# Performance work log

Measured on AMD Instinct MI355X. Metric: run time of the kernel, lower is better.

The kernel has to match this reference:

```python
import jax, jax.numpy as jnp
import numpy as np

EMBED_DIM = 1024
NUM_HEADS = 16
HEAD_DIM = EMBED_DIM // NUM_HEADS


def setup_inputs() -> dict:
    key = jax.random.key(0)
    ks = jax.random.split(key, 9)
    s = 1.0 / np.sqrt(EMBED_DIM)
    x = jax.random.normal(ks[0], (2, 2048, EMBED_DIM), dtype=jnp.float32)
    Wq = jax.random.uniform(ks[1], (EMBED_DIM, EMBED_DIM), jnp.float32, -s, s)
    bq = jax.random.uniform(ks[2], (EMBED_DIM,), jnp.float32, -s, s)
    Wk = jax.random.uniform(ks[3], (EMBED_DIM, EMBED_DIM), jnp.float32, -s, s)
    bk = jax.random.uniform(ks[4], (EMBED_DIM,), jnp.float32, -s, s)
    Wv = jax.random.uniform(ks[5], (EMBED_DIM, EMBED_DIM), jnp.float32, -s, s)
    bv = jax.random.uniform(ks[6], (EMBED_DIM,), jnp.float32, -s, s)
    Wo = jax.random.uniform(ks[7], (EMBED_DIM, EMBED_DIM), jnp.float32, -s, s)
    bo = jax.random.uniform(ks[8], (EMBED_DIM,), jnp.float32, -s, s)
    return {"x": x, "Wq": Wq, "bq": bq, "Wk": Wk, "bk": bk,
            "Wv": Wv, "bv": bv, "Wo": Wo, "bo": bo}


def reference(x, Wq, bq, Wk, bk, Wv, bv, Wo, bo):
    B, N, C = x.shape
    H, D = NUM_HEADS, HEAD_DIM
    # nn.Linear: y = x @ W.T + b; here W stored as [in, out] so y = x @ W + b
    def split_heads(y):
        return y.reshape(B, N, H, D).transpose(0, 2, 1, 3)  # [B,H,N,D]
    q = split_heads(x @ Wq + bq)
    k = split_heads(x @ Wk + bk)
    v = split_heads(x @ Wv + bv)
    scores = jnp.einsum('bhnd,bhmd->bhnm', q, k) / jnp.sqrt(jnp.float32(D)).astype(x.dtype)
    attn = jax.nn.softmax(scores, axis=-1)
    ctx = jnp.einsum('bhnm,bhmd->bhnd', attn, v)
    ctx = ctx.transpose(0, 2, 1, 3).reshape(B, N, C)
    return ctx @ Wo + bo
```

## Files before the change

kernel.cpp:

```cpp
#include <hip/hip_runtime.h>
#include <hip/hip_bf16.h>
#include <stdint.h>
#include <stddef.h>

using bf16 = __hip_bfloat16;
using bf16x8 = __attribute__((ext_vector_type(8))) short;
using f32x4  = __attribute__((ext_vector_type(4))) float;
using f32x16 = __attribute__((ext_vector_type(16))) float;
typedef unsigned int u32x2 __attribute__((ext_vector_type(2)));
typedef unsigned int u32x4 __attribute__((ext_vector_type(4)));

#define MFMA16(a, b, c) __builtin_amdgcn_mfma_f32_16x16x32_bf16((a), (b), (c), 0, 0, 0)
#define MFMA32(a, b, c) __builtin_amdgcn_mfma_f32_32x32x16_bf16((a), (b), (c), 0, 0, 0)

#define GLD16(g, l)                                                            \
  __builtin_amdgcn_global_load_lds(                                            \
      (const __attribute__((address_space(1))) void*)(g),                      \
      (__attribute__((address_space(3))) void*)(l), 16, 0, 0)

__device__ __forceinline__ float exp2_fast(float x) {
#if __has_builtin(__builtin_amdgcn_exp2f)
  return __builtin_amdgcn_exp2f(x);
#else
  return __expf(x * 0.69314718056f);
#endif
}

__device__ __forceinline__ float fmax3(float a, float b, float c) {
  return fmaxf(fmaxf(a, b), c);
}

__device__ __forceinline__ unsigned int cvtpk_bf16(float lo, float hi) {
  unsigned int r;
  asm("v_cvt_pk_bf16_f32 %0, %1, %2" : "=v"(r) : "v"(lo), "v"(hi));
  return r;
}

__device__ __forceinline__ void permswap(unsigned int& a, unsigned int& b, int hi) {
#if __has_builtin(__builtin_amdgcn_permlane32_swap)
  u32x2 r = __builtin_amdgcn_permlane32_swap(a, b, false, false);
  a = r.x;
  b = r.y;
#else
  unsigned int sa = __shfl_xor((unsigned int)a, 32, 64);
  unsigned int sb = __shfl_xor((unsigned int)b, 32, 64);
  unsigned int an = hi ? sb : a;
  unsigned int bn = hi ? b : sa;
  a = an; b = bn;
#endif
}


__global__ void convert_x(const float* __restrict__ x, bf16* __restrict__ out) {
  const int i = blockIdx.x * 256 + threadIdx.x;
  const float4 v = ((const float4*)x)[i];
  __hip_bfloat162* o2 = (__hip_bfloat162*)(out + (size_t)i * 4);
  o2[0] = __float22bfloat162_rn(make_float2(v.x, v.y));
  o2[1] = __float22bfloat162_rn(make_float2(v.z, v.w));
}

__global__ void convert_w(const float* __restrict__ W0, const float* __restrict__ W1,
                          const float* __restrict__ W2, const float* __restrict__ W3,
                          bf16* __restrict__ Wt) {
  __shared__ float t[32][33];
  const int bx = blockIdx.x;
  const int mat = bx >> 10;
  const float* W = (mat == 0) ? W0 : (mat == 1) ? W1 : (mat == 2) ? W2 : W3;
  const int rem = bx & 1023;
  const int k0 = (rem >> 5) * 32, n0 = (rem & 31) * 32;
  const int c = threadIdx.x & 31, r0 = (threadIdx.x >> 5) * 4;
#pragma unroll
  for (int i = 0; i < 4; ++i) {
    const int r = r0 + i;
    t[r][c] = W[(size_t)(k0 + r) * 1024 + n0 + c];
  }
  __syncthreads();
  bf16* dst = Wt + (size_t)mat * 1024 * 1024;
#pragma unroll
  for (int i = 0; i < 4; ++i) {
    const int rn = r0 + i;
    dst[(size_t)(n0 + rn) * 1024 + k0 + c] = __float2bfloat16(t[c][rn]);
  }
}

__global__ void concat_bias(const float* __restrict__ bq, const float* __restrict__ bk,
                            const float* __restrict__ bv, const float* __restrict__ bo,
                            float* __restrict__ dst) {
  const int i = blockIdx.x * 256 + threadIdx.x;
  const float* src = (i < 1024) ? bq : (i < 2048) ? bk : (i < 3072) ? bv : bo;
  dst[i] = src[i & 1023];
}

__global__ __launch_bounds__(512, 2)
void gemm_qkv(const bf16* __restrict__ A, const bf16* __restrict__ Bt,
              const float* __restrict__ bias,
              bf16* __restrict__ Qb, bf16* __restrict__ Kf, bf16* __restrict__ Vf) {
  __shared__ bf16 Ab[2][128 * 64];
  __shared__ bf16 Bb[2][384 * 64];
  const int tid = threadIdx.x;
  const int lane = tid & 63, w = tid >> 6;
  const int wr = w >> 2, wc = w & 3;
  const int lrow = lane & 15, lgk = lane >> 4;

  const int bid = blockIdx.x;
  const int xcd = bid & 7, i5 = bid >> 3;
  const int xr = xcd >> 1, xc = xcd & 1;
  const int bm = (xr * 8 + (i5 & 7)) * 128;
  const int bn = (xc * 4 + (i5 >> 3)) * 384;

  f32x4 acc[4][6] = {};

  auto stageA = [&](int b, int kt) {
#pragma unroll
    for (int v = 0; v < 2; ++v) {
      const int c = v * 512 + tid;
      const int r = c >> 3, j = c & 7;
      GLD16(A + (size_t)(bm + r) * 1024 + kt * 64 + ((j ^ (r & 7)) * 8),
            &Ab[b][c * 8]);
    }
  };
  auto stageB = [&](int b, int kt, int u) {
#pragma unroll
    for (int v = 0; v < 2; ++v) {
      const int cl = v * 512 + tid;
      const int r = u * 128 + (cl >> 3), j = cl & 7;
      GLD16(Bt + (size_t)(bn + r) * 1024 + kt * 64 + ((j ^ ((r & 7))) * 8),
            &Bb[b][(r * 8 + (j)) * 8]);
    }
  };

  auto readA = [&](int b, bf16x8 (&dst)[8]) {
#pragma unroll
    for (int mf = 0; mf < 4; ++mf)
#pragma unroll
      for (int kk = 0; kk < 2; ++kk) {
        const int r = wr * 64 + mf * 16 + lrow;
        const int s = (kk * 4 + lgk) ^ (r & 7);
        dst[mf * 2 + kk] = *(const bf16x8*)(&Ab[b][(r * 8 + s) * 8]);
      }
  };
  auto readB2 = [&](int b, int nf0, bf16x8 (&dst)[4]) {
#pragma unroll
    for (int nf = 0; nf < 2; ++nf)
#pragma unroll
      for (int kk = 0; kk < 2; ++kk) {
        const int r = wc * 96 + (nf0 + nf) * 16 + lrow;
        const int s = (kk * 4 + lgk) ^ (r & 7);
        dst[nf * 2 + kk] = *(const bf16x8*)(&Bb[b][(r * 8 + s) * 8]);
      }
  };

  stageA(0, 0);
  stageB(0, 0, 0);
  stageB(0, 0, 1);
  stageB(0, 0, 2);
  stageA(1, 1);
  asm volatile("s_waitcnt vmcnt(2)" ::: "memory");
  __builtin_amdgcn_s_barrier();

  bf16x8 a_[8], b01[4], b23[4], b45[4];

  for (int t = 0; t < 16; ++t) {
    const int b = t & 1, nb = b ^ 1;
    if (t < 15) {
      stageB(nb, t + 1, 0);
      stageB(nb, t + 1, 1);
    }
    readA(b, a_);
    readB2(b, 0, b01);
    asm volatile("s_waitcnt lgkmcnt(0)" ::: "memory");
    __builtin_amdgcn_sched_barrier(0);
    __builtin_amdgcn_s_setprio(1);
#pragma unroll
    for (int mf = 0; mf < 4; ++mf)
#pragma unroll
      for (int nf = 0; nf < 2; ++nf)
#pragma unroll
        for (int kk = 0; kk < 2; ++kk)
          acc[mf][nf] = MFMA16(a_[mf * 2 + kk], b01[nf * 2 + kk], acc[mf][nf]);
    __builtin_amdgcn_s_setprio(0);
    if (t < 15) stageB(nb, t + 1, 2);
    readB2(b, 2, b23);
    asm volatile("s_waitcnt lgkmcnt(0)" ::: "memory");
    __builtin_amdgcn_sched_barrier(0);
    __builtin_amdgcn_s_setprio(1);
#pragma unroll
    for (int mf = 0; mf < 4; ++mf)
#pragma unroll
      for (int nf = 0; nf < 2; ++nf)
#pragma unroll
        for (int kk = 0; kk < 2; ++kk)
          acc[mf][2 + nf] = MFMA16(a_[mf * 2 + kk], b23[nf * 2 + kk], acc[mf][2 + nf]);
    __builtin_amdgcn_s_setprio(0);
    readB2(b, 4, b45);
    asm volatile("s_waitcnt lgkmcnt(0)" ::: "memory");
    __builtin_amdgcn_sched_barrier(0);
    __builtin_amdgcn_s_barrier();
    if (t < 14) stageA(b, t + 2);
    __builtin_amdgcn_s_setprio(1);
#pragma unroll
    for (int mf = 0; mf < 4; ++mf)
#pragma unroll
      for (int nf = 0; nf < 2; ++nf)
#pragma unroll
        for (int kk = 0; kk < 2; ++kk)
          acc[mf][4 + nf] = MFMA16(a_[mf * 2 + kk], b45[nf * 2 + kk], acc[mf][4 + nf]);
    __builtin_amdgcn_s_setprio(0);
    if (t < 14)
      asm volatile("s_waitcnt vmcnt(2)" ::: "memory");
    else
      asm volatile("s_waitcnt vmcnt(0)" ::: "memory");
    __builtin_amdgcn_s_barrier();
  }

#pragma unroll
  for (int mf = 0; mf < 4; ++mf) {
#pragma unroll
    for (int nf = 0; nf < 6; ++nf) {
      const int col = bn + wc * 96 + nf * 16 + lrow;
      const float bv_ = bias[col];
      const int row0 = bm + wr * 64 + mf * 16 + lgk * 4;
      const int which = col >> 10;
      const int hd = col & 1023;
      const int h = hd >> 6, d = hd & 63;
      const int bb = row0 >> 11, t0 = row0 & 2047;
      const int bh = bb * 16 + h;
      const int tt = (t0 >> 6) & 31;
      if (which == 2) {
        const int ks = (t0 >> 4) & 3, vhi = (t0 >> 3) & 1, e0 = t0 & 7;
        const int dt = d >> 5, lo5 = d & 31;
        bf16* vp = Vf + (((size_t)bh * 32 + tt) * 8 + dt * 4 + ks) * 512 +
                   (vhi * 32 + lo5) * 8 + e0;
        uint2 pk;
        pk.x = cvtpk_bf16(acc[mf][nf][0] + bv_, acc[mf][nf][1] + bv_);
        pk.y = cvtpk_bf16(acc[mf][nf][2] + bv_, acc[mf][nf][3] + bv_);
        *(uint2*)vp = pk;
      } else if (which == 0) {
#pragma unroll
        for (int j = 0; j < 4; ++j)
          Qb[((size_t)bh * 2048 + t0 + j) * 64 + d] =
              __float2bfloat16((acc[mf][nf][j] + bv_) * 0.18033688f);
      } else {
        const int kt = (t0 >> 5) & 1, lo5 = t0 & 31;
        const int f = d >> 4, khi = (d >> 3) & 1, e = d & 7;
        bf16* kp = Kf + (((size_t)bh * 32 + tt) * 8 + kt * 4 + f) * 512 +
                   (khi * 32 + lo5) * 8 + e;
#pragma unroll
        for (int j = 0; j < 4; ++j)
          kp[j * 8] = __float2bfloat16(acc[mf][nf][j] + bv_);
      }
    }
  }
}

__global__ __launch_bounds__(256)
void gemm_o(const bf16* __restrict__ A, const bf16* __restrict__ Bt,
            const float* __restrict__ bias, float* __restrict__ Of, int K) {
  __shared__ bf16 As[3][128 * 32];
  __shared__ bf16 Bs[3][64 * 32];
  const int tid = threadIdx.x;
  const int lane = tid & 63, w = tid >> 6;
  const int wr = w >> 1, wc = w & 1;
  const int lrow = lane & 15, lgk = lane >> 4;
  const int bm = blockIdx.y * 128, bn = blockIdx.x * 64;
  f32x4 acc[4][2] = {};
  const bf16* Ab = A + (size_t)bm * K;
  const bf16* Bb = Bt + (size_t)bn * K;
  const int e0 = tid, e1 = 256 + tid;
  const int NT = K >> 5;

  auto stage = [&](int s, int k0) {
    GLD16(Ab + (size_t)(e0 >> 2) * K + k0 + (e0 & 3) * 8, &As[s][e0 * 8]);
    GLD16(Ab + (size_t)(e1 >> 2) * K + k0 + (e1 & 3) * 8, &As[s][e1 * 8]);
    GLD16(Bb + (size_t)(e0 >> 2) * K + k0 + (e0 & 3) * 8, &Bs[s][e0 * 8]);
  };

  stage(0, 0);
  stage(1, 32);
  int cur = 0, nxt = 2;
  for (int t = 0; t < NT; ++t) {
    if (t < NT - 1)
      asm volatile("s_waitcnt vmcnt(3)" ::: "memory");
    else
      asm volatile("s_waitcnt vmcnt(0)" ::: "memory");
    __builtin_amdgcn_s_barrier();
    if (t + 2 < NT) {
      stage(nxt, (t + 2) << 5);
      nxt = (nxt == 2) ? 0 : nxt + 1;
    }
    bf16x8 af[4], bfr[2];
#pragma unroll
    for (int m = 0; m < 4; ++m)
      af[m] = *(const bf16x8*)(&As[cur][(wr * 64 + m * 16 + lrow) * 32 + lgk * 8]);
#pragma unroll
    for (int n = 0; n < 2; ++n)
      bfr[n] = *(const bf16x8*)(&Bs[cur][(wc * 32 + n * 16 + lrow) * 32 + lgk * 8]);
#pragma unroll
    for (int m = 0; m < 4; ++m)
#pragma unroll
      for (int n = 0; n < 2; ++n)
        acc[m][n] = MFMA16(af[m], bfr[n], acc[m][n]);
    cur = (cur == 2) ? 0 : cur + 1;
  }

#pragma unroll
  for (int m = 0; m < 4; ++m) {
#pragma unroll
    for (int n = 0; n < 2; ++n) {
      const int col = bn + wc * 32 + n * 16 + lrow;
      const float bv_ = bias[col];
      const int row0 = bm + wr * 64 + m * 16 + lgk * 4;
#pragma unroll
      for (int j = 0; j < 4; ++j)
        Of[(size_t)(row0 + j) * 1024 + col] = acc[m][n][j] + bv_;
    }
  }
}

__global__ __launch_bounds__(256, 2)
void attn_kernel(const bf16* __restrict__ Q, const bf16* __restrict__ Kf,
                 const bf16* __restrict__ Vf, bf16* __restrict__ ctx) {
  const int tid = threadIdx.x, lane = tid & 63, w = tid >> 6;
  const int lo5 = lane & 31, hi = lane >> 5;

  const int bid = blockIdx.x;
  const int xcd = bid & 7, idx = bid >> 3;
  const int bh = (xcd << 2) | (idx >> 4);
  const int qt = idx & 15;
  const int q0 = qt * 128 + w * 32;

  const bf16* Qbh = Q + (size_t)bh * 2048 * 64;
  const bf16* Kp = Kf + (size_t)bh * 32 * 4096 + lane * 8;
  const bf16* Vp = Vf + (size_t)bh * 32 * 4096 + lane * 8;

  bf16x8 qf[4];
#pragma unroll
  for (int f = 0; f < 4; ++f)
    qf[f] = *(const bf16x8*)(Qbh + (size_t)(q0 + lo5) * 64 + f * 16 + hi * 8);

  f32x16 o0 = {}, o1 = {};
  float m2 = -1e30f;
  float lsum = 0.f;
  bf16x8 pa[4];

  auto softmax_pa = [&](f32x16& s0, f32x16& s1) {
    float r1[11];
#pragma unroll
    for (int i = 0; i < 5; ++i)
      r1[i] = fmax3(s0[3 * i], s0[3 * i + 1], s0[3 * i + 2]);
    r1[5] = fmax3(s0[15], s1[0], s1[1]);
#pragma unroll
    for (int i = 0; i < 4; ++i)
      r1[6 + i] = fmax3(s1[2 + 3 * i], s1[3 + 3 * i], s1[4 + 3 * i]);
    r1[10] = fmaxf(s1[14], s1[15]);
    float r2[4];
#pragma unroll
    for (int i = 0; i < 3; ++i) r2[i] = fmax3(r1[3 * i], r1[3 * i + 1], r1[3 * i + 2]);
    r2[3] = fmaxf(r1[9], r1[10]);
    const float pm = fmaxf(fmax3(r2[0], r2[1], r2[2]), r2[3]);
    if (!__all(pm <= m2 + 11.5416f)) {
      const float mx = fmaxf(pm, __shfl_xor(pm, 32, 64));
      const float mn = fmaxf(m2, mx);
      const float corr = exp2_fast(m2 - mn);
      m2 = mn;
      lsum *= corr;
#pragma unroll
      for (int j = 0; j < 16; ++j) { o0[j] *= corr; o1[j] *= corr; }
    }
#pragma unroll
    for (int j = 0; j < 16; ++j) s0[j] = exp2_fast(s0[j] - m2);
#pragma unroll
    for (int j = 0; j < 16; ++j) s1[j] = exp2_fast(s1[j] - m2);
    float a8[8];
#pragma unroll
    for (int j = 0; j < 8; ++j) a8[j] = (s0[j] + s0[j + 8]) + (s1[j] + s1[j + 8]);
    float a4[4];
#pragma unroll
    for (int j = 0; j < 4; ++j) a4[j] = a8[j] + a8[j + 4];
    lsum += (a4[0] + a4[1]) + (a4[2] + a4[3]);
#pragma unroll
    for (int ks = 0; ks < 4; ++ks) {
      const f32x16& s = (ks < 2) ? s0 : s1;
      const int b0 = (ks & 1) * 8;
      unsigned int a0 = cvtpk_bf16(s[b0 + 0], s[b0 + 1]);
      unsigned int c0 = cvtpk_bf16(s[b0 + 4], s[b0 + 5]);
      unsigned int a1 = cvtpk_bf16(s[b0 + 2], s[b0 + 3]);
      unsigned int c1 = cvtpk_bf16(s[b0 + 6], s[b0 + 7]);
      permswap(a0, c0, hi);
      permswap(a1, c1, hi);
      u32x4 tt;
      tt.x = a0; tt.y = a1; tt.z = c0; tt.w = c1;
      pa[ks] = __builtin_bit_cast(bf16x8, tt);
    }
  };

  bf16x8 kA[8], kB[8], vb[8];

  auto loadK = [&](int t, bf16x8 (&kb)[8]) {
    const bf16* p = Kp + (size_t)t * 4096;
#pragma unroll
    for (int fi = 0; fi < 8; ++fi) kb[fi] = *(const bf16x8*)(p + fi * 512);
  };
  auto loadV = [&](int t) {
    const bf16* p = Vp + (size_t)t * 4096;
#pragma unroll
    for (int fi = 0; fi < 8; ++fi) vb[fi] = *(const bf16x8*)(p + fi * 512);
  };

  loadK(0, kA);

  auto step = [&](int t, bf16x8 (&kc)[8], bf16x8 (&kn)[8]) {
    loadV(t);
    if (t < 31) loadK(t + 1, kn);
    f32x16 s0 = {}, s1 = {};
#pragma unroll
    for (int f = 0; f < 4; ++f) s0 = MFMA32(kc[f], qf[f], s0);
#pragma unroll
    for (int f = 0; f < 4; ++f) s1 = MFMA32(kc[4 + f], qf[f], s1);
    softmax_pa(s0, s1);
#pragma unroll
    for (int ks = 0; ks < 4; ++ks) {
      o0 = MFMA32(vb[ks], pa[ks], o0);
      o1 = MFMA32(vb[4 + ks], pa[ks], o1);
    }
  };

  for (int t = 0; t < 32; t += 2) {
    step(t, kA, kB);
    step(t + 1, kB, kA);
  }

  lsum += __shfl_xor(lsum, 32, 64);
  const float inv = 1.f / lsum;
  const int b = bh >> 4, h = bh & 15;
  bf16* crow = ctx + (size_t)(b * 2048 + q0 + lo5) * 1024 + h * 64;
#pragma unroll
  for (int g = 0; g < 4; ++g) {
    uint2 pk0, pk1;
    pk0.x = cvtpk_bf16(o0[4 * g + 0] * inv, o0[4 * g + 1] * inv);
    pk0.y = cvtpk_bf16(o0[4 * g + 2] * inv, o0[4 * g + 3] * inv);
    pk1.x = cvtpk_bf16(o1[4 * g + 0] * inv, o1[4 * g + 1] * inv);
    pk1.y = cvtpk_bf16(o1[4 * g + 2] * inv, o1[4 * g + 3] * inv);
    *(uint2*)(crow + 8 * g + 4 * hi) = pk0;
    *(uint2*)(crow + 32 + 8 * g + 4 * hi) = pk1;
  }
}


extern "C" void kernel_launch(void* const* d_in, const int* in_sizes, int n_in,
                              void* d_out, int out_size, void* d_ws, size_t ws_size,
                              hipStream_t stream) {
  const float* x  = (const float*)d_in[0];
  const float* Wq = (const float*)d_in[1];
  const float* bq = (const float*)d_in[2];
  const float* Wk = (const float*)d_in[3];
  const float* bk = (const float*)d_in[4];
  const float* Wv = (const float*)d_in[5];
  const float* bv = (const float*)d_in[6];
  const float* Wo = (const float*)d_in[7];
  const float* bo = (const float*)d_in[8];
  float* out = (float*)d_out;

  char* ws = (char*)d_ws;
  bf16* xb  = (bf16*)(ws);
  bf16* Wt  = (bf16*)(ws + ((size_t)8 << 20));
  bf16* Qb  = (bf16*)(ws + ((size_t)16 << 20));
  bf16* Kf  = (bf16*)(ws + ((size_t)24 << 20));
  bf16* Vf  = (bf16*)(ws + ((size_t)32 << 20));
  bf16* ctx = (bf16*)(ws + ((size_t)40 << 20));
  float* ba = (float*)(ws + ((size_t)48 << 20));

  convert_x<<<dim3(4096), dim3(256), 0, stream>>>(x, xb);
  convert_w<<<dim3(4096), dim3(256), 0, stream>>>(Wq, Wk, Wv, Wo, Wt);
  concat_bias<<<dim3(16), dim3(256), 0, stream>>>(bq, bk, bv, bo, ba);

  gemm_qkv<<<dim3(256), dim3(512), 0, stream>>>(xb, Wt, ba, Qb, Kf, Vf);

  attn_kernel<<<dim3(512), dim3(256), 0, stream>>>(Qb, Kf, Vf, ctx);

  gemm_o<<<dim3(16, 32), dim3(256), 0, stream>>>(
      ctx, Wt + (size_t)3072 * 1024, ba + 3072, out, 1024);
}
```

Baseline: 122.8 us.

## Split attention KV loop across two wave teams with LDS softmax merge

The attention kernel now runs 8 waves per block. Two teams of four waves each process half of the key/value tiles for the same query rows. Team 1 writes its partial output, running max and sum to shared memory, and team 0 merges them with flash-style rescaling before writing the context. This doubles parallelism per block to hide the latency of the serial KV loop. The cost is about 35KB of LDS per block, a block barrier, and tighter register limits from launch_bounds(512,4).

```diff
diff --git a/kernel.cpp b/kernel.cpp
--- a/kernel.cpp
+++ b/kernel.cpp
@@ -317,21 +317,25 @@
   }
 }
 
-__global__ __launch_bounds__(256, 2)
+__global__ __launch_bounds__(512, 4)
 void attn_kernel(const bf16* __restrict__ Q, const bf16* __restrict__ Kf,
                  const bf16* __restrict__ Vf, bf16* __restrict__ ctx) {
+  __shared__ float mbuf[4][64][34];
+
   const int tid = threadIdx.x, lane = tid & 63, w = tid >> 6;
   const int lo5 = lane & 31, hi = lane >> 5;
+  const int team = w >> 2, wq = w & 3;
 
   const int bid = blockIdx.x;
   const int xcd = bid & 7, idx = bid >> 3;
   const int bh = (xcd << 2) | (idx >> 4);
   const int qt = idx & 15;
-  const int q0 = qt * 128 + w * 32;
+  const int q0 = qt * 128 + wq * 32;
 
   const bf16* Qbh = Q + (size_t)bh * 2048 * 64;
   const bf16* Kp = Kf + (size_t)bh * 32 * 4096 + lane * 8;
   const bf16* Vp = Vf + (size_t)bh * 32 * 4096 + lane * 8;
+  const int tg0 = team * 16;
 
   bf16x8 qf[4];
 #pragma unroll
@@ -407,11 +411,11 @@
     for (int fi = 0; fi < 8; ++fi) vb[fi] = *(const bf16x8*)(p + fi * 512);
   };
 
-  loadK(0, kA);
+  loadK(tg0, kA);
 
   auto step = [&](int t, bf16x8 (&kc)[8], bf16x8 (&kn)[8]) {
-    loadV(t);
-    if (t < 31) loadK(t + 1, kn);
+    loadV(tg0 + t);
+    if (t < 15) loadK(tg0 + t + 1, kn);
     f32x16 s0 = {}, s1 = {};
 #pragma unroll
     for (int f = 0; f < 4; ++f) s0 = MFMA32(kc[f], qf[f], s0);
@@ -425,24 +429,46 @@
     }
   };
 
-  for (int t = 0; t < 32; t += 2) {
+  for (int t = 0; t < 16; t += 2) {
     step(t, kA, kB);
     step(t + 1, kB, kA);
   }
 
-  lsum += __shfl_xor(lsum, 32, 64);
-  const float inv = 1.f / lsum;
-  const int b = bh >> 4, h = bh & 15;
-  bf16* crow = ctx + (size_t)(b * 2048 + q0 + lo5) * 1024 + h * 64;
-#pragma unroll
-  for (int g = 0; g < 4; ++g) {
-    uint2 pk0, pk1;
-    pk0.x = cvtpk_bf16(o0[4 * g + 0] * inv, o0[4 * g + 1] * inv);
-    pk0.y = cvtpk_bf16(o0[4 * g + 2] * inv, o0[4 * g + 3] * inv);
-    pk1.x = cvtpk_bf16(o1[4 * g + 0] * inv, o1[4 * g + 1] * inv);
-    pk1.y = cvtpk_bf16(o1[4 * g + 2] * inv, o1[4 * g + 3] * inv);
-    *(uint2*)(crow + 8 * g + 4 * hi) = pk0;
-    *(uint2*)(crow + 32 + 8 * g + 4 * hi) = pk1;
+  if (team == 1) {
+    float* dst = &mbuf[wq][lane][0];
+#pragma unroll
+    for (int j = 0; j < 16; ++j) dst[j] = o0[j];
+#pragma unroll
+    for (int j = 0; j < 16; ++j) dst[16 + j] = o1[j];
+    dst[32] = m2;
+    dst[33] = lsum;
+  }
+  __syncthreads();
+  if (team == 0) {
+    const float* src = &mbuf[wq][lane][0];
+    const float m2B = src[32], lB = src[33];
+    const float m = fmaxf(m2, m2B);
+    const float cA = exp2_fast(m2 - m), cB = exp2_fast(m2B - m);
+    lsum = lsum * cA + lB * cB;
+#pragma unroll
+    for (int j = 0; j < 16; ++j) o0[j] = o0[j] * cA + src[j] * cB;
+#pragma unroll
+    for (int j = 0; j < 16; ++j) o1[j] = o1[j] * cA + src[16 + j] * cB;
+
+    lsum += __shfl_xor(lsum, 32, 64);
+    const float inv = 1.f / lsum;
+    const int b = bh >> 4, h = bh & 15;
+    bf16* crow = ctx + (size_t)(b * 2048 + q0 + lo5) * 1024 + h * 64;
+#pragma unroll
+    for (int g = 0; g < 4; ++g) {
+      uint2 pk0, pk1;
+      pk0.x = cvtpk_bf16(o0[4 * g + 0] * inv, o0[4 * g + 1] * inv);
+      pk0.y = cvtpk_bf16(o0[4 * g + 2] * inv, o0[4 * g + 3] * inv);
+      pk1.x = cvtpk_bf16(o1[4 * g + 0] * inv, o1[4 * g + 1] * inv);
+      pk1.y = cvtpk_bf16(o1[4 * g + 2] * inv, o1[4 * g + 3] * inv);
+      *(uint2*)(crow + 8 * g + 4 * hi) = pk0;
+      *(uint2*)(crow + 32 + 8 * g + 4 * hi) = pk1;
+    }
   }
 }
 
@@ -476,7 +502,7 @@
 
   gemm_qkv<<<dim3(256), dim3(512), 0, stream>>>(xb, Wt, ba, Qb, Kf, Vf);
 
-  attn_kernel<<<dim3(512), dim3(256), 0, stream>>>(Qb, Kf, Vf, ctx);
+  attn_kernel<<<dim3(512), dim3(512), 0, stream>>>(Qb, Kf, Vf, ctx);
 
   gemm_o<<<dim3(16, 32), dim3(256), 0, stream>>>(
       ctx, Wt + (size_t)3072 * 1024, ba + 3072, out, 1024);
```

Result: slower. 300.9 us (+145.0%).

## Double-buffer K and V tiles with inline-asm loads and manual vmcnt waits

Applied to the files above, without the earlier changes.

Attention K/V loads now go through inline-asm global_load_dwordx4, two tiles ahead, with double buffers for both K and V. Explicit s_waitcnt vmcnt counts and sched barriers replace the compiler's waits, so the loads for tile t+2 are issued after tile t is consumed. Before, V was loaded in the same step that used it, which exposed load latency. This raises register pressure (four tile buffers), so the launch bound drops the min-blocks-per-CU hint, which may lower occupancy. Hand-written waitcnt is also fragile if the compiler emits other memory ops.

```diff
diff --git a/kernel.cpp b/kernel.cpp
--- a/kernel.cpp
+++ b/kernel.cpp
@@ -317,7 +317,7 @@
   }
 }
 
-__global__ __launch_bounds__(256, 2)
+__global__ __launch_bounds__(256)
 void attn_kernel(const bf16* __restrict__ Q, const bf16* __restrict__ Kf,
                  const bf16* __restrict__ Vf, bf16* __restrict__ ctx) {
   const int tid = threadIdx.x, lane = tid & 63, w = tid >> 6;
@@ -329,14 +329,58 @@
   const int qt = idx & 15;
   const int q0 = qt * 128 + w * 32;
 
-  const bf16* Qbh = Q + (size_t)bh * 2048 * 64;
+  const bf16* Qp = Q + (size_t)bh * 2048 * 64 + (size_t)(q0 + lo5) * 64 + hi * 8;
   const bf16* Kp = Kf + (size_t)bh * 32 * 4096 + lane * 8;
   const bf16* Vp = Vf + (size_t)bh * 32 * 4096 + lane * 8;
 
   bf16x8 qf[4];
-#pragma unroll
-  for (int f = 0; f < 4; ++f)
-    qf[f] = *(const bf16x8*)(Qbh + (size_t)(q0 + lo5) * 64 + f * 16 + hi * 8);
+  asm volatile(
+      "global_load_dwordx4 %0, %4, off\n\t"
+      "global_load_dwordx4 %1, %4, off offset:32\n\t"
+      "global_load_dwordx4 %2, %4, off offset:64\n\t"
+      "global_load_dwordx4 %3, %4, off offset:96"
+      : "=v"(qf[0]), "=v"(qf[1]), "=v"(qf[2]), "=v"(qf[3])
+      : "v"(Qp)
+      : "memory");
+
+  bf16x8 kA[8], vA[8], kB[8], vB[8];
+
+#define ISSUE_TILE(t, kb, vbuf_)                                               \
+  {                                                                            \
+    const bf16* pk = Kp + (size_t)(t) * 4096;                                  \
+    const bf16* pv = Vp + (size_t)(t) * 4096;                                  \
+    asm volatile(                                                              \
+        "global_load_dwordx4 %0, %8, off\n\t"                                  \
+        "global_load_dwordx4 %1, %8, off offset:1024\n\t"                      \
+        "global_load_dwordx4 %2, %8, off offset:2048\n\t"                      \
+        "global_load_dwordx4 %3, %8, off offset:3072\n\t"                      \
+        "global_load_dwordx4 %4, %9, off\n\t"                                  \
+        "global_load_dwordx4 %5, %9, off offset:1024\n\t"                      \
+        "global_load_dwordx4 %6, %9, off offset:2048\n\t"                      \
+        "global_load_dwordx4 %7, %9, off offset:3072"                          \
+        : "=v"(kb[0]), "=v"(kb[1]), "=v"(kb[2]), "=v"(kb[3]),                  \
+          "=v"(kb[4]), "=v"(kb[5]), "=v"(kb[6]), "=v"(kb[7])                   \
+        : "v"(pk), "v"(pk + 2048)                                              \
+        : "memory");                                                           \
+    asm volatile(                                                              \
+        "global_load_dwordx4 %0, %8, off\n\t"                                  \
+        "global_load_dwordx4 %1, %8, off offset:1024\n\t"                      \
+        "global_load_dwordx4 %2, %8, off offset:2048\n\t"                      \
+        "global_load_dwordx4 %3, %8, off offset:3072\n\t"                      \
+        "global_load_dwordx4 %4, %9, off\n\t"                                  \
+        "global_load_dwordx4 %5, %9, off offset:1024\n\t"                      \
+        "global_load_dwordx4 %6, %9, off offset:2048\n\t"                      \
+        "global_load_dwordx4 %7, %9, off offset:3072"                          \
+        : "=v"(vbuf_[0]), "=v"(vbuf_[1]), "=v"(vbuf_[2]), "=v"(vbuf_[3]),      \
+          "=v"(vbuf_[4]), "=v"(vbuf_[5]), "=v"(vbuf_[6]), "=v"(vbuf_[7])       \
+        : "v"(pv), "v"(pv + 2048)                                              \
+        : "memory");                                                           \
+  }
+
+  ISSUE_TILE(0, kA, vA);
+  ISSUE_TILE(1, kB, vB);
+  asm volatile("s_waitcnt vmcnt(32)" ::: "memory");
+  __builtin_amdgcn_sched_barrier(0);
 
   f32x16 o0 = {}, o1 = {};
   float m2 = -1e30f;
@@ -394,24 +438,12 @@
     }
   };
 
-  bf16x8 kA[8], kB[8], vb[8];
-
-  auto loadK = [&](int t, bf16x8 (&kb)[8]) {
-    const bf16* p = Kp + (size_t)t * 4096;
-#pragma unroll
-    for (int fi = 0; fi < 8; ++fi) kb[fi] = *(const bf16x8*)(p + fi * 512);
-  };
-  auto loadV = [&](int t) {
-    const bf16* p = Vp + (size_t)t * 4096;
-#pragma unroll
-    for (int fi = 0; fi < 8; ++fi) vb[fi] = *(const bf16x8*)(p + fi * 512);
-  };
-
-  loadK(0, kA);
-
-  auto step = [&](int t, bf16x8 (&kc)[8], bf16x8 (&kn)[8]) {
-    loadV(t);
-    if (t < 31) loadK(t + 1, kn);
+  auto step = [&](int t, bf16x8 (&kc)[8], bf16x8 (&vc)[8]) {
+    if (t < 31)
+      asm volatile("s_waitcnt vmcnt(16)" ::: "memory");
+    else
+      asm volatile("s_waitcnt vmcnt(0)" ::: "memory");
+    __builtin_amdgcn_sched_barrier(0);
     f32x16 s0 = {}, s1 = {};
 #pragma unroll
     for (int f = 0; f < 4; ++f) s0 = MFMA32(kc[f], qf[f], s0);
@@ -420,14 +452,15 @@
     softmax_pa(s0, s1);
 #pragma unroll
     for (int ks = 0; ks < 4; ++ks) {
-      o0 = MFMA32(vb[ks], pa[ks], o0);
-      o1 = MFMA32(vb[4 + ks], pa[ks], o1);
-    }
+      o0 = MFMA32(vc[ks], pa[ks], o0);
+      o1 = MFMA32(vc[4 + ks], pa[ks], o1);
+    }
+    if (t + 2 < 32) ISSUE_TILE(t + 2, kc, vc);
   };
 
   for (int t = 0; t < 32; t += 2) {
-    step(t, kA, kB);
-    step(t + 1, kB, kA);
+    step(t, kA, vA);
+    step(t + 1, kB, vB);
   }
 
   lsum += __shfl_xor(lsum, 32, 64);
```

Result: no change. 122.8 us (+0.0%).
